# Optimization experiments

Hardware: AMD Instinct MI355X
Metric: run time of the kernel (lower is better)

Reference implementation:

```python
import jax, jax.numpy as jnp
import numpy as np

N_NODES = 50000
N_EDGES = 800000
N_REL = 4
D_IN = 128
D_OUT = 128


def setup_inputs() -> dict:
    key = jax.random.key(0)
    ks = jax.random.split(key, 7)
    X = jax.random.normal(ks[0], (N_NODES, D_IN), dtype=jnp.float32)
    rows = jax.random.randint(ks[1], (N_REL, N_EDGES), 0, N_NODES, dtype=jnp.int64)
    cols = jax.random.randint(ks[2], (N_REL, N_EDGES), 0, N_NODES, dtype=jnp.int64)
    vals = jax.random.uniform(ks[3], (N_REL, N_EDGES), dtype=jnp.float32)
    W_rel = jax.random.normal(ks[4], (N_REL, D_IN, D_OUT), dtype=jnp.float32) * (1.0 / np.sqrt(D_IN))
    W_self = jax.random.normal(ks[5], (D_IN, D_OUT), dtype=jnp.float32) * (1.0 / np.sqrt(D_IN))
    bias = jax.random.normal(ks[6], (D_OUT,), dtype=jnp.float32) * 0.01
    return {"X": X, "rows": rows, "cols": cols, "vals": vals,
            "W_rel": W_rel, "W_self": W_self, "bias": bias}


def reference(X, rows, cols, vals, W_rel, W_self, bias):
    """MedGCN multi-relation graph conv: out = X@W_self + sum_r norm(A_r)@X@W_r + b.

    Each A_r given as COO edge list (rows[r], cols[r], vals[r]); duplicate
    indices are summed (matching torch coalesce semantics).
    """
    n = X.shape[0]
    out = X @ W_self + bias
    for r in range(W_rel.shape[0]):
        i, j, v = rows[r], cols[r], vals[r]
        # D^{-1/2} A D^{-1/2}: deg[i] = sum_j A[i, j]
        deg = jax.ops.segment_sum(v, i, num_segments=n)
        inv_sqrt = jnp.clip(deg, 1e-12) ** -0.5
        v_norm = v * inv_sqrt[i] * inv_sqrt[j]
        # spmm: (A_norm @ X)[i] = sum over edges with row i of v_norm * X[j]
        AX = jax.ops.segment_sum(v_norm[:, None] * X[j], i, num_segments=n)
        out = out + AX @ W_rel[r]
    return out
```

## Files before the change

kernel.cpp:

```cpp
#include <hip/hip_runtime.h>
#include <hip/hip_bf16.h>

#define N_NODES 50000
#define N_EDGES 800000
#define N_REL   4
#define D       128
#define NE      (N_REL * N_EDGES)

#define S_SEG   64
#define SEG_E   (NE / S_SEG)
#define G_RANGES 8
#define RPG     (N_NODES / G_RANGES)

#define NCNT    (N_NODES * S_SEG)
#define SCAN_CHUNK 4096
#define NBLK ((NCNT + SCAN_CHUNK - 1) / SCAN_CHUNK)

#define OFF_BST   0
#define OFF_BSUM  12800000
#define OFF_BOFF  12803200
#define OFF_EREC  12806400
#define OFF_Y     38406400
#define OFF_RANK  89606400
#define OFF_INV2  96006400

typedef __attribute__((ext_vector_type(8))) short bf16x8;
typedef __attribute__((ext_vector_type(4))) float f32x4;

__device__ inline unsigned short f2bf(float f) {
    unsigned u = __float_as_uint(f);
    u += 0x7fffu + ((u >> 16) & 1u);
    return (unsigned short)(u >> 16);
}

__global__ __launch_bounds__(256) void k_prep_w(const float* __restrict__ Wself,
                                                const float* __restrict__ Wrel,
                                                unsigned short* __restrict__ Wt) {
    int id = blockIdx.x * 256 + threadIdx.x;
    int seg = id >> 14;
    int rem = id & 16383;
    int n = rem >> 7, k = rem & 127;
    float v = (seg == 0) ? Wself[k * 128 + n] : Wrel[(size_t)(seg - 1) * 16384 + k * 128 + n];
    Wt[id] = f2bf(v);
}

__global__ __launch_bounds__(256) void k_mm(const float* __restrict__ X,
                                            const unsigned short* __restrict__ Wt,
                                            const float* __restrict__ bias,
                                            float* __restrict__ out,
                                            unsigned short* __restrict__ Yb) {
    const int m0 = blockIdx.x * 64;
    const int tid = threadIdx.x;
    const int wave = tid >> 6, lane = tid & 63;
    const int wm = wave >> 1, wn = wave & 1;

    __shared__ unsigned short Xs[64][136];

#pragma unroll
    for (int l = 0; l < 8; l++) {
        int c = tid + l * 256;
        int row = c >> 5, c4 = c & 31;
        int gr = m0 + row;
        float4 v = make_float4(0.f, 0.f, 0.f, 0.f);
        if (gr < N_NODES) v = *(const float4*)(X + (size_t)gr * 128 + c4 * 4);
        ushort4 h;
        h.x = f2bf(v.x); h.y = f2bf(v.y); h.z = f2bf(v.z); h.w = f2bf(v.w);
        *(ushort4*)&Xs[row][c4 * 4] = h;
    }
    __syncthreads();

    const int lr = lane & 15;
    const int kb = (lane >> 4) * 8;
    const int lrow = (lane >> 4) * 4;
    const int lcol = lane & 15;
    const f32x4 zero = {0.f, 0.f, 0.f, 0.f};

    for (int seg = 0; seg < 5; seg++) {
        const unsigned short* Wseg = Wt + (size_t)seg * 16384;
        f32x4 acc[2][4];
#pragma unroll
        for (int i = 0; i < 2; i++)
#pragma unroll
            for (int j = 0; j < 4; j++) acc[i][j] = zero;

#pragma unroll
        for (int k0 = 0; k0 < 128; k0 += 32) {
            bf16x8 a[2], b[4];
#pragma unroll
            for (int i = 0; i < 2; i++)
                a[i] = *(const bf16x8*)&Xs[wm * 32 + i * 16 + lr][k0 + kb];
#pragma unroll
            for (int j = 0; j < 4; j++)
                b[j] = *(const bf16x8*)(Wseg + (size_t)(wn * 64 + j * 16 + lr) * 128 + k0 + kb);
#pragma unroll
            for (int i = 0; i < 2; i++)
#pragma unroll
                for (int j = 0; j < 4; j++)
                    acc[i][j] = __builtin_amdgcn_mfma_f32_16x16x32_bf16(a[i], b[j], acc[i][j], 0, 0, 0);
        }

        if (seg == 0) {
#pragma unroll
            for (int i = 0; i < 2; i++) {
#pragma unroll
                for (int j = 0; j < 4; j++) {
                    int gc = wn * 64 + j * 16 + lcol;
                    float bv = bias[gc];
#pragma unroll
                    for (int v = 0; v < 4; v++) {
                        int gr = m0 + wm * 32 + i * 16 + lrow + v;
                        if (gr < N_NODES)
                            out[(size_t)gr * 128 + gc] = acc[i][j][v] + bv;
                    }
                }
            }
        } else {
            unsigned short* Yseg = Yb + (size_t)(seg - 1) * N_NODES * 128;
#pragma unroll
            for (int i = 0; i < 2; i++) {
#pragma unroll
                for (int j = 0; j < 4; j++) {
                    int gc = wn * 64 + j * 16 + lcol;
#pragma unroll
                    for (int v = 0; v < 4; v++) {
                        int gr = m0 + wm * 32 + i * 16 + lrow + v;
                        if (gr < N_NODES)
                            Yseg[(size_t)gr * 128 + gc] = f2bf(acc[i][j][v]);
                    }
                }
            }
        }
    }
}

__global__ __launch_bounds__(256) void k_count(const int* __restrict__ rows,
                                               int* __restrict__ cntt,
                                               unsigned short* __restrict__ rank) {
    __shared__ int lc[RPG];
    const int seg = blockIdx.x >> 3;
    const int g = blockIdx.x & 7;
    const int rbase = g * RPG;
    for (int i = threadIdx.x; i < RPG; i += 256) lc[i] = 0;
    __syncthreads();
    const int4* r4 = (const int4*)(rows + (size_t)seg * SEG_E);
    const int n4 = SEG_E / 4;
    for (int i = threadIdx.x; i < n4; i += 256) {
        int4 v = r4[i];
        int t = seg * SEG_E + i * 4;
        unsigned int l0 = (unsigned int)(v.x - rbase);
        unsigned int l1 = (unsigned int)(v.y - rbase);
        unsigned int l2 = (unsigned int)(v.z - rbase);
        unsigned int l3 = (unsigned int)(v.w - rbase);
        if (l0 < (unsigned int)RPG) rank[t]     = (unsigned short)atomicAdd(&lc[l0], 1);
        if (l1 < (unsigned int)RPG) rank[t + 1] = (unsigned short)atomicAdd(&lc[l1], 1);
        if (l2 < (unsigned int)RPG) rank[t + 2] = (unsigned short)atomicAdd(&lc[l2], 1);
        if (l3 < (unsigned int)RPG) rank[t + 3] = (unsigned short)atomicAdd(&lc[l3], 1);
    }
    __syncthreads();
    for (int i = threadIdx.x; i < RPG; i += 256)
        cntt[(size_t)seg * N_NODES + rbase + i] = lc[i];
}

__global__ __launch_bounds__(256) void k_tr(const int* __restrict__ cntt,
                                            int* __restrict__ bst) {
    __shared__ int tile[64][65];
    const int r0 = blockIdx.x * 64;
    const int l = threadIdx.x & 63;
    const int q = threadIdx.x >> 6;
#pragma unroll
    for (int p = 0; p < 16; ++p) {
        int seg = q * 16 + p;
        int row = r0 + l;
        tile[seg][l] = (row < N_NODES) ? cntt[(size_t)seg * N_NODES + row] : 0;
    }
    __syncthreads();
#pragma unroll
    for (int p = 0; p < 16; ++p) {
        int rr = q * 16 + p;
        int row = r0 + rr;
        if (row < N_NODES) bst[(size_t)row * S_SEG + l] = tile[l][rr];
    }
}

__global__ __launch_bounds__(256) void k_scanA(int* __restrict__ bst,
                                               int* __restrict__ bsum) {
    __shared__ int s[256];
    int t = threadIdx.x;
    int base = blockIdx.x * SCAN_CHUNK + t * 16;
    int4 v[4];
    int tsum = 0;
#pragma unroll
    for (int q = 0; q < 4; ++q) {
        int idx = base + q * 4;
        if (idx < NCNT) v[q] = *(const int4*)(bst + idx);
        else v[q] = make_int4(0, 0, 0, 0);
        tsum += v[q].x + v[q].y + v[q].z + v[q].w;
    }
    s[t] = tsum;
    __syncthreads();
    for (int off = 1; off < 256; off <<= 1) {
        int x = (t >= off) ? s[t - off] : 0;
        __syncthreads();
        s[t] += x;
        __syncthreads();
    }
    int run = s[t] - tsum;
#pragma unroll
    for (int q = 0; q < 4; ++q) {
        int idx = base + q * 4;
        if (idx < NCNT) {
            int4 o;
            o.x = run; run += v[q].x;
            o.y = run; run += v[q].y;
            o.z = run; run += v[q].z;
            o.w = run; run += v[q].w;
            *(int4*)(bst + idx) = o;
        }
    }
    if (t == 255) bsum[blockIdx.x] = s[255];
}

__global__ __launch_bounds__(256) void k_scanB(const int* __restrict__ bsum,
                                               int* __restrict__ boff) {
    __shared__ int s[256];
    int t = threadIdx.x;
    int b = t * 4;
    int v0 = (b     < NBLK) ? bsum[b]     : 0;
    int v1 = (b + 1 < NBLK) ? bsum[b + 1] : 0;
    int v2 = (b + 2 < NBLK) ? bsum[b + 2] : 0;
    int v3 = (b + 3 < NBLK) ? bsum[b + 3] : 0;
    int tsum = v0 + v1 + v2 + v3;
    s[t] = tsum;
    __syncthreads();
    for (int off = 1; off < 256; off <<= 1) {
        int x = (t >= off) ? s[t - off] : 0;
        __syncthreads();
        s[t] += x;
        __syncthreads();
    }
    int excl = s[t] - tsum;
    if (b     < NBLK) boff[b]     = excl;
    if (b + 1 < NBLK) boff[b + 1] = excl + v0;
    if (b + 2 < NBLK) boff[b + 2] = excl + v0 + v1;
    if (b + 3 < NBLK) boff[b + 3] = excl + v0 + v1 + v2;
}

__global__ __launch_bounds__(256) void k_scanC(int* __restrict__ bst,
                                               const int* __restrict__ boff) {
    int t = threadIdx.x;
    int base = blockIdx.x * SCAN_CHUNK + t * 16;
    int add = boff[blockIdx.x];
#pragma unroll
    for (int q = 0; q < 4; ++q) {
        int idx = base + q * 4;
        if (idx < NCNT) {
            int4 v = *(const int4*)(bst + idx);
            v.x += add; v.y += add; v.z += add; v.w += add;
            *(int4*)(bst + idx) = v;
        }
    }
}

__global__ __launch_bounds__(256) void k_fill(const int* __restrict__ rows,
                                              const int* __restrict__ cols,
                                              const float* __restrict__ vals,
                                              const int* __restrict__ bst,
                                              const unsigned short* __restrict__ rank,
                                              int2* __restrict__ erec) {
    int t = blockIdx.x * 256 + threadIdx.x;
    if (t >= NE) return;
    int seg = t / SEG_E;
    int r = seg >> 4;
    int row = rows[t], col = cols[t];
    int pos = bst[(size_t)row * S_SEG + seg] + (int)rank[t];
    erec[pos] = make_int2(r * N_NODES + col, __float_as_int(vals[t]));
}

__global__ __launch_bounds__(256) void k_deg(const int* __restrict__ bst,
                                             const int2* __restrict__ erec,
                                             float* __restrict__ inv2) {
    int t = blockIdx.x * 256 + threadIdx.x;
    if (t >= N_NODES * 4) return;
    int row = t >> 2, rel = t & 3;
    int s = bst[(size_t)row * S_SEG + rel * 16];
    int e = (rel < 3) ? bst[(size_t)row * S_SEG + rel * 16 + 16]
                      : ((row + 1 < N_NODES) ? bst[(size_t)(row + 1) * S_SEG] : NE);
    float acc = 0.f;
    for (int i = s; i < e; ++i) acc += __int_as_float(erec[i].y);
    inv2[t] = rsqrtf(fmaxf(acc, 1e-12f));
}

__global__ __launch_bounds__(256, 8) void k_gather(const int* __restrict__ bst,
                                                   const int2* __restrict__ erec,
                                                   const float* __restrict__ inv2,
                                                   const unsigned int* __restrict__ Y2,
                                                   float* __restrict__ out) {
    const int wid = threadIdx.x >> 6;
    const int lane = threadIdx.x & 63;
    const int row = blockIdx.x * 4 + wid;
    if (row >= N_NODES) return;

    const int start = bst[(size_t)row * S_SEG];
    const int end = (row + 1 < N_NODES) ? bst[(size_t)(row + 1) * S_SEG] : NE;
    const float4 sv = *(const float4*)(inv2 + (size_t)row * 4);

    float ax = 0.f, ay = 0.f;
    for (int base = start; base < end; base += 64) {
        const int rem = end - base;
        int pcL = 0;
        float cfL = 0.f;
        if (lane < rem) {
            int2 rec = erec[base + lane];
            int pc = rec.x;
            int r = (int)((unsigned int)pc / (unsigned int)N_NODES);
            int col = pc - r * N_NODES;
            float selfinv = (r == 0) ? sv.x : (r == 1) ? sv.y : (r == 2) ? sv.z : sv.w;
            cfL = __int_as_float(rec.y) * selfinv * inv2[(size_t)col * 4 + r];
            pcL = pc;
        }
        if (rem >= 64) {
#pragma unroll
            for (int i = 0; i < 64; ++i) {
                int pc = __builtin_amdgcn_readlane(pcL, i);
                float cf = __int_as_float(__builtin_amdgcn_readlane(__float_as_int(cfL), i));
                unsigned int y = Y2[(size_t)pc * 64 + lane];
                ax = fmaf(cf, __uint_as_float(y << 16), ax);
                ay = fmaf(cf, __uint_as_float(y & 0xffff0000u), ay);
            }
        } else {
            for (int i = 0; i < rem; ++i) {
                int pc = __builtin_amdgcn_readlane(pcL, i);
                float cf = __int_as_float(__builtin_amdgcn_readlane(__float_as_int(cfL), i));
                unsigned int y = Y2[(size_t)pc * 64 + lane];
                ax = fmaf(cf, __uint_as_float(y << 16), ax);
                ay = fmaf(cf, __uint_as_float(y & 0xffff0000u), ay);
            }
        }
    }
    float2* op = (float2*)(out + (size_t)row * D) + lane;
    float2 o = *op;
    o.x += ax;
    o.y += ay;
    *op = o;
}

extern "C" void kernel_launch(void* const* d_in, const int* in_sizes, int n_in,
                              void* d_out, int out_size, void* d_ws, size_t ws_size,
                              hipStream_t stream) {
    const float* X     = (const float*)d_in[0];
    const int*   rows  = (const int*)d_in[1];
    const int*   cols  = (const int*)d_in[2];
    const float* vals  = (const float*)d_in[3];
    const float* Wrel  = (const float*)d_in[4];
    const float* Wself = (const float*)d_in[5];
    const float* bias  = (const float*)d_in[6];
    float* out = (float*)d_out;

    char* ws = (char*)d_ws;
    int*   bst  = (int*)(ws + OFF_BST);
    int*   bsum = (int*)(ws + OFF_BSUM);
    int*   boff = (int*)(ws + OFF_BOFF);
    int2*  erec = (int2*)(ws + OFF_EREC);
    int*   cntt = (int*)(ws + OFF_EREC);
    unsigned short* Wt = (unsigned short*)(ws + OFF_EREC);
    unsigned short* Yb = (unsigned short*)(ws + OFF_Y);
    unsigned short* rank = (unsigned short*)(ws + OFF_RANK);
    float* inv2 = (float*)(ws + OFF_INV2);

    k_prep_w<<<320, 256, 0, stream>>>(Wself, Wrel, Wt);

    k_mm<<<(N_NODES + 63) / 64, 256, 0, stream>>>(X, Wt, bias, out, Yb);

    k_count<<<S_SEG * G_RANGES, 256, 0, stream>>>(rows, cntt, rank);
    k_tr<<<(N_NODES + 63) / 64, 256, 0, stream>>>(cntt, bst);
    k_scanA<<<NBLK, 256, 0, stream>>>(bst, bsum);
    k_scanB<<<1, 256, 0, stream>>>(bsum, boff);
    k_scanC<<<NBLK, 256, 0, stream>>>(bst, boff);

    k_fill<<<(NE + 255) / 256, 256, 0, stream>>>(rows, cols, vals, bst, rank, erec);
    k_deg<<<(N_NODES * 4 + 255) / 256, 256, 0, stream>>>(bst, erec, inv2);
    k_gather<<<(N_NODES + 3) / 4, 256, 0, stream>>>(bst, erec, inv2,
                                                    (const unsigned int*)Yb, out);
}
```

Measured before the change: 368.1 us.

## Aggregate neighbor features first, then fuse all relations into one K=640 GEMM

Reorders the computation from (X·W_r) then gather to gather-X-first. Each relation's normalized A_r·X is written as bf16 into a concatenated [X | A_0X | … | A_3X] buffer, followed by a single GEMM with a stacked 640×128 weight. This drops the separate transformed-feature arrays and the read-modify-write of the output, and makes the random-gather footprint a single bf16 copy of X. The cost is that the gather now loops per relation with short edge runs, which tend to hit the non-unrolled tail path, and the GEMM has a larger K. Workspace buffers are re-aliased to fit.

```diff
diff --git a/kernel.cpp b/kernel.cpp
--- a/kernel.cpp
+++ b/kernel.cpp
@@ -17,12 +17,9 @@
 #define NBLK ((NCNT + SCAN_CHUNK - 1) / SCAN_CHUNK)
 
 #define OFF_BST   0
-#define OFF_BSUM  12800000
-#define OFF_BOFF  12803200
-#define OFF_EREC  12806400
-#define OFF_Y     38406400
-#define OFF_RANK  89606400
-#define OFF_INV2  96006400
+#define OFF_INV2  12800000
+#define OFF_EREC  13600000
+#define OFF_AXC   39200000
 
 typedef __attribute__((ext_vector_type(8))) short bf16x8;
 typedef __attribute__((ext_vector_type(4))) float f32x4;
@@ -31,106 +28,6 @@
     unsigned u = __float_as_uint(f);
     u += 0x7fffu + ((u >> 16) & 1u);
     return (unsigned short)(u >> 16);
-}
-
-__global__ __launch_bounds__(256) void k_prep_w(const float* __restrict__ Wself,
-                                                const float* __restrict__ Wrel,
-                                                unsigned short* __restrict__ Wt) {
-    int id = blockIdx.x * 256 + threadIdx.x;
-    int seg = id >> 14;
-    int rem = id & 16383;
-    int n = rem >> 7, k = rem & 127;
-    float v = (seg == 0) ? Wself[k * 128 + n] : Wrel[(size_t)(seg - 1) * 16384 + k * 128 + n];
-    Wt[id] = f2bf(v);
-}
-
-__global__ __launch_bounds__(256) void k_mm(const float* __restrict__ X,
-                                            const unsigned short* __restrict__ Wt,
-                                            const float* __restrict__ bias,
-                                            float* __restrict__ out,
-                                            unsigned short* __restrict__ Yb) {
-    const int m0 = blockIdx.x * 64;
-    const int tid = threadIdx.x;
-    const int wave = tid >> 6, lane = tid & 63;
-    const int wm = wave >> 1, wn = wave & 1;
-
-    __shared__ unsigned short Xs[64][136];
-
-#pragma unroll
-    for (int l = 0; l < 8; l++) {
-        int c = tid + l * 256;
-        int row = c >> 5, c4 = c & 31;
-        int gr = m0 + row;
-        float4 v = make_float4(0.f, 0.f, 0.f, 0.f);
-        if (gr < N_NODES) v = *(const float4*)(X + (size_t)gr * 128 + c4 * 4);
-        ushort4 h;
-        h.x = f2bf(v.x); h.y = f2bf(v.y); h.z = f2bf(v.z); h.w = f2bf(v.w);
-        *(ushort4*)&Xs[row][c4 * 4] = h;
-    }
-    __syncthreads();
-
-    const int lr = lane & 15;
-    const int kb = (lane >> 4) * 8;
-    const int lrow = (lane >> 4) * 4;
-    const int lcol = lane & 15;
-    const f32x4 zero = {0.f, 0.f, 0.f, 0.f};
-
-    for (int seg = 0; seg < 5; seg++) {
-        const unsigned short* Wseg = Wt + (size_t)seg * 16384;
-        f32x4 acc[2][4];
-#pragma unroll
-        for (int i = 0; i < 2; i++)
-#pragma unroll
-            for (int j = 0; j < 4; j++) acc[i][j] = zero;
-
-#pragma unroll
-        for (int k0 = 0; k0 < 128; k0 += 32) {
-            bf16x8 a[2], b[4];
-#pragma unroll
-            for (int i = 0; i < 2; i++)
-                a[i] = *(const bf16x8*)&Xs[wm * 32 + i * 16 + lr][k0 + kb];
-#pragma unroll
-            for (int j = 0; j < 4; j++)
-                b[j] = *(const bf16x8*)(Wseg + (size_t)(wn * 64 + j * 16 + lr) * 128 + k0 + kb);
-#pragma unroll
-            for (int i = 0; i < 2; i++)
-#pragma unroll
-                for (int j = 0; j < 4; j++)
-                    acc[i][j] = __builtin_amdgcn_mfma_f32_16x16x32_bf16(a[i], b[j], acc[i][j], 0, 0, 0);
-        }
-
-        if (seg == 0) {
-#pragma unroll
-            for (int i = 0; i < 2; i++) {
-#pragma unroll
-                for (int j = 0; j < 4; j++) {
-                    int gc = wn * 64 + j * 16 + lcol;
-                    float bv = bias[gc];
-#pragma unroll
-                    for (int v = 0; v < 4; v++) {
-                        int gr = m0 + wm * 32 + i * 16 + lrow + v;
-                        if (gr < N_NODES)
-                            out[(size_t)gr * 128 + gc] = acc[i][j][v] + bv;
-                    }
-                }
-            }
-        } else {
-            unsigned short* Yseg = Yb + (size_t)(seg - 1) * N_NODES * 128;
-#pragma unroll
-            for (int i = 0; i < 2; i++) {
-#pragma unroll
-                for (int j = 0; j < 4; j++) {
-                    int gc = wn * 64 + j * 16 + lcol;
-#pragma unroll
-                    for (int v = 0; v < 4; v++) {
-                        int gr = m0 + wm * 32 + i * 16 + lrow + v;
-                        if (gr < N_NODES)
-                            Yseg[(size_t)gr * 128 + gc] = f2bf(acc[i][j][v]);
-                    }
-                }
-            }
-        }
-    }
 }
 
 __global__ __launch_bounds__(256) void k_count(const int* __restrict__ rows,
@@ -270,10 +167,9 @@
     int t = blockIdx.x * 256 + threadIdx.x;
     if (t >= NE) return;
     int seg = t / SEG_E;
-    int r = seg >> 4;
     int row = rows[t], col = cols[t];
     int pos = bst[(size_t)row * S_SEG + seg] + (int)rank[t];
-    erec[pos] = make_int2(r * N_NODES + col, __float_as_int(vals[t]));
+    erec[pos] = make_int2(col, __float_as_int(vals[t]));
 }
 
 __global__ __launch_bounds__(256) void k_deg(const int* __restrict__ bst,
@@ -290,58 +186,146 @@
     inv2[t] = rsqrtf(fmaxf(acc, 1e-12f));
 }
 
-__global__ __launch_bounds__(256, 8) void k_gather(const int* __restrict__ bst,
-                                                   const int2* __restrict__ erec,
-                                                   const float* __restrict__ inv2,
-                                                   const unsigned int* __restrict__ Y2,
-                                                   float* __restrict__ out) {
+__global__ __launch_bounds__(256) void k_prep_x(const float* __restrict__ X,
+                                                unsigned short* __restrict__ AXc) {
+    int id = blockIdx.x * 256 + threadIdx.x;
+    int row = id >> 5, c4 = id & 31;
+    float4 v = *(const float4*)(X + (size_t)row * 128 + c4 * 4);
+    ushort4 h;
+    h.x = f2bf(v.x); h.y = f2bf(v.y); h.z = f2bf(v.z); h.w = f2bf(v.w);
+    *(ushort4*)(AXc + (size_t)row * 640 + c4 * 4) = h;
+}
+
+__global__ __launch_bounds__(256) void k_prep_w(const float* __restrict__ Wself,
+                                                const float* __restrict__ Wrel,
+                                                unsigned short* __restrict__ Wt2) {
+    int id = blockIdx.x * 256 + threadIdx.x;
+    int n = id / 640;
+    int k = id - n * 640;
+    float v;
+    if (k < 128) v = Wself[k * 128 + n];
+    else {
+        int r = (k - 128) >> 7, kk = (k - 128) & 127;
+        v = Wrel[((size_t)r * 128 + kk) * 128 + n];
+    }
+    Wt2[(size_t)n * 640 + k] = f2bf(v);
+}
+
+__global__ __launch_bounds__(256, 8) void k_gax(const int* __restrict__ bst,
+                                                const int2* __restrict__ erec,
+                                                const float* __restrict__ inv2,
+                                                unsigned int* __restrict__ AXu) {
     const int wid = threadIdx.x >> 6;
     const int lane = threadIdx.x & 63;
     const int row = blockIdx.x * 4 + wid;
     if (row >= N_NODES) return;
 
-    const int start = bst[(size_t)row * S_SEG];
-    const int end = (row + 1 < N_NODES) ? bst[(size_t)(row + 1) * S_SEG] : NE;
-    const float4 sv = *(const float4*)(inv2 + (size_t)row * 4);
-
-    float ax = 0.f, ay = 0.f;
-    for (int base = start; base < end; base += 64) {
-        const int rem = end - base;
-        int pcL = 0;
-        float cfL = 0.f;
-        if (lane < rem) {
-            int2 rec = erec[base + lane];
-            int pc = rec.x;
-            int r = (int)((unsigned int)pc / (unsigned int)N_NODES);
-            int col = pc - r * N_NODES;
-            float selfinv = (r == 0) ? sv.x : (r == 1) ? sv.y : (r == 2) ? sv.z : sv.w;
-            cfL = __int_as_float(rec.y) * selfinv * inv2[(size_t)col * 4 + r];
-            pcL = pc;
-        }
-        if (rem >= 64) {
-#pragma unroll
-            for (int i = 0; i < 64; ++i) {
-                int pc = __builtin_amdgcn_readlane(pcL, i);
-                float cf = __int_as_float(__builtin_amdgcn_readlane(__float_as_int(cfL), i));
-                unsigned int y = Y2[(size_t)pc * 64 + lane];
-                ax = fmaf(cf, __uint_as_float(y << 16), ax);
-                ay = fmaf(cf, __uint_as_float(y & 0xffff0000u), ay);
+    const int bend = (row + 1 < N_NODES) ? bst[(size_t)(row + 1) * S_SEG] : NE;
+
+    for (int rel = 0; rel < 4; rel++) {
+        const float selfinv = inv2[(size_t)row * 4 + rel];
+        const int s = bst[(size_t)row * S_SEG + rel * 16];
+        const int e = (rel < 3) ? bst[(size_t)row * S_SEG + rel * 16 + 16] : bend;
+        float ax0 = 0.f, ay0 = 0.f;
+        for (int base = s; base < e; base += 64) {
+            const int rem = e - base;
+            int pcL = 0;
+            float cfL = 0.f;
+            if (lane < rem) {
+                int2 rec = erec[base + lane];
+                pcL = rec.x;
+                cfL = __int_as_float(rec.y) * selfinv * inv2[(size_t)rec.x * 4 + rel];
             }
-        } else {
-            for (int i = 0; i < rem; ++i) {
-                int pc = __builtin_amdgcn_readlane(pcL, i);
-                float cf = __int_as_float(__builtin_amdgcn_readlane(__float_as_int(cfL), i));
-                unsigned int y = Y2[(size_t)pc * 64 + lane];
-                ax = fmaf(cf, __uint_as_float(y << 16), ax);
-                ay = fmaf(cf, __uint_as_float(y & 0xffff0000u), ay);
+            if (rem >= 64) {
+#pragma unroll
+                for (int i = 0; i < 64; ++i) {
+                    int pc = __builtin_amdgcn_readlane(pcL, i);
+                    float cf = __int_as_float(__builtin_amdgcn_readlane(__float_as_int(cfL), i));
+                    unsigned int y = AXu[(size_t)pc * 320 + lane];
+                    ax0 = fmaf(cf, __uint_as_float(y << 16), ax0);
+                    ay0 = fmaf(cf, __uint_as_float(y & 0xffff0000u), ay0);
+                }
+            } else {
+                for (int i = 0; i < rem; ++i) {
+                    int pc = __builtin_amdgcn_readlane(pcL, i);
+                    float cf = __int_as_float(__builtin_amdgcn_readlane(__float_as_int(cfL), i));
+                    unsigned int y = AXu[(size_t)pc * 320 + lane];
+                    ax0 = fmaf(cf, __uint_as_float(y << 16), ax0);
+                    ay0 = fmaf(cf, __uint_as_float(y & 0xffff0000u), ay0);
+                }
             }
         }
-    }
-    float2* op = (float2*)(out + (size_t)row * D) + lane;
-    float2 o = *op;
-    o.x += ax;
-    o.y += ay;
-    *op = o;
+        unsigned int lo = f2bf(ax0);
+        unsigned int hi = f2bf(ay0);
+        AXu[(size_t)row * 320 + 64 + rel * 64 + lane] = (hi << 16) | lo;
+    }
+}
+
+__global__ __launch_bounds__(256) void k_mm2(const unsigned short* __restrict__ AXc,
+                                             const unsigned short* __restrict__ Wt2,
+                                             const float* __restrict__ bias,
+                                             float* __restrict__ out) {
+    const int m0 = blockIdx.x * 128;
+    const int tid = threadIdx.x;
+    const int wave = tid >> 6, lane = tid & 63;
+    const int wm = wave >> 1, wn = wave & 1;
+
+    __shared__ unsigned short As[128][40];
+
+    const f32x4 zero = {0.f, 0.f, 0.f, 0.f};
+    f32x4 acc[4][4];
+#pragma unroll
+    for (int i = 0; i < 4; i++)
+#pragma unroll
+        for (int j = 0; j < 4; j++) acc[i][j] = zero;
+
+    const int lr = lane & 15;
+    const int kb = (lane >> 4) * 8;
+
+    for (int k0 = 0; k0 < 640; k0 += 32) {
+#pragma unroll
+        for (int l = 0; l < 2; l++) {
+            int id = tid + l * 256;
+            int row = id >> 2, c4 = id & 3;
+            int gr = m0 + row;
+            int4 v = make_int4(0, 0, 0, 0);
+            if (gr < N_NODES)
+                v = *(const int4*)(AXc + (size_t)gr * 640 + k0 + c4 * 8);
+            *(int4*)&As[row][c4 * 8] = v;
+        }
+        __syncthreads();
+
+        bf16x8 a[4], b[4];
+#pragma unroll
+        for (int i = 0; i < 4; i++)
+            a[i] = *(const bf16x8*)&As[wm * 64 + i * 16 + lr][kb];
+#pragma unroll
+        for (int j = 0; j < 4; j++)
+            b[j] = *(const bf16x8*)(Wt2 + (size_t)(wn * 64 + j * 16 + lr) * 640 + k0 + kb);
+#pragma unroll
+        for (int i = 0; i < 4; i++)
+#pragma unroll
+            for (int j = 0; j < 4; j++)
+                acc[i][j] = __builtin_amdgcn_mfma_f32_16x16x32_bf16(a[i], b[j], acc[i][j], 0, 0, 0);
+        __syncthreads();
+    }
+
+    const int lrow = (lane >> 4) * 4;
+    const int lcol = lane & 15;
+#pragma unroll
+    for (int i = 0; i < 4; i++) {
+#pragma unroll
+        for (int j = 0; j < 4; j++) {
+            int gc = wn * 64 + j * 16 + lcol;
+            float bv = bias[gc];
+#pragma unroll
+            for (int v = 0; v < 4; v++) {
+                int gr = m0 + wm * 64 + i * 16 + lrow + v;
+                if (gr < N_NODES)
+                    out[(size_t)gr * 128 + gc] = acc[i][j][v] + bv;
+            }
+        }
+    }
 }
 
 extern "C" void kernel_launch(void* const* d_in, const int* in_sizes, int n_in,
@@ -358,27 +342,27 @@
 
     char* ws = (char*)d_ws;
     int*   bst  = (int*)(ws + OFF_BST);
-    int*   bsum = (int*)(ws + OFF_BSUM);
-    int*   boff = (int*)(ws + OFF_BOFF);
+    float* inv2 = (float*)(ws + OFF_INV2);
     int2*  erec = (int2*)(ws + OFF_EREC);
     int*   cntt = (int*)(ws + OFF_EREC);
-    unsigned short* Wt = (unsigned short*)(ws + OFF_EREC);
-    unsigned short* Yb = (unsigned short*)(ws + OFF_Y);
-    unsigned short* rank = (unsigned short*)(ws + OFF_RANK);
-    float* inv2 = (float*)(ws + OFF_INV2);
-
-    k_prep_w<<<320, 256, 0, stream>>>(Wself, Wrel, Wt);
-
-    k_mm<<<(N_NODES + 63) / 64, 256, 0, stream>>>(X, Wt, bias, out, Yb);
+    unsigned short* AXc = (unsigned short*)(ws + OFF_AXC);
+    unsigned short* rank = (unsigned short*)(ws + OFF_AXC);
+    int*   bsum = (int*)(ws + OFF_AXC + 6400000);
+    int*   boff = (int*)(ws + OFF_AXC + 6403200);
+    unsigned short* Wt2 = (unsigned short*)(ws + OFF_BST);
 
     k_count<<<S_SEG * G_RANGES, 256, 0, stream>>>(rows, cntt, rank);
     k_tr<<<(N_NODES + 63) / 64, 256, 0, stream>>>(cntt, bst);
     k_scanA<<<NBLK, 256, 0, stream>>>(bst, bsum);
     k_scanB<<<1, 256, 0, stream>>>(bsum, boff);
     k_scanC<<<NBLK, 256, 0, stream>>>(bst, boff);
-
     k_fill<<<(NE + 255) / 256, 256, 0, stream>>>(rows, cols, vals, bst, rank, erec);
     k_deg<<<(N_NODES * 4 + 255) / 256, 256, 0, stream>>>(bst, erec, inv2);
-    k_gather<<<(N_NODES + 3) / 4, 256, 0, stream>>>(bst, erec, inv2,
-                                                    (const unsigned int*)Yb, out);
-}
+
+    k_prep_x<<<6250, 256, 0, stream>>>(X, AXc);
+    k_gax<<<(N_NODES + 3) / 4, 256, 0, stream>>>(bst, erec, inv2,
+                                                 (unsigned int*)AXc);
+
+    k_prep_w<<<320, 256, 0, stream>>>(Wself, Wrel, Wt2);
+    k_mm2<<<(N_NODES + 127) / 128, 256, 0, stream>>>(AXc, Wt2, bias, out);
+}
```

Measured after the change: 404.3 us. 9.8% more time.
